# Kernel optimization log

Hardware: AMD Instinct MI355X
Metric: run time of the kernel (lower is better)

The kernel has to match this reference:

```python
import jax, jax.numpy as jnp
import numpy as np

N, E, L, HEADS, HID = 50000, 600000, 4, 8, 128
IN_C, OUT_C = 64, 64
D_HEAD = HID // HEADS


def _layer_norm(x, g, b, eps=1e-5):
    m = jnp.mean(x, axis=-1, keepdims=True)
    v = jnp.mean((x - m) ** 2, axis=-1, keepdims=True)
    return (x - m) * jax.lax.rsqrt(v + eps) * g + b


def _transformer_conv(h, src, dst, Wq, bq, Wk, bk, Wv, bv, Ws, bs, Wbeta):
    # PyG TransformerConv with beta=True, concat=True. src=edge_index[0] (j), dst=edge_index[1] (i).
    n, f = h.shape
    q = (h @ Wq.T + bq)[dst].reshape(-1, HEADS, D_HEAD)   # [E,H,D] query at destination
    k = (h @ Wk.T + bk)[src].reshape(-1, HEADS, D_HEAD)   # [E,H,D] key at source
    v = (h @ Wv.T + bv)[src].reshape(-1, HEADS, D_HEAD)   # [E,H,D] value at source
    alpha = jnp.sum(q * k, axis=-1) / float(np.sqrt(D_HEAD))  # [E,H]
    amax = jax.ops.segment_max(alpha, dst, num_segments=n)     # [N,H] segment softmax (stable)
    ex = jnp.exp(alpha - amax[dst])
    denom = jax.ops.segment_sum(ex, dst, num_segments=n)
    a = ex / (denom[dst] + 1e-16)                              # [E,H]
    out = jax.ops.segment_sum((a[:, :, None] * v).reshape(-1, f), dst, num_segments=n)  # [N,F]
    x_r = h @ Ws.T + bs                                        # root/skip transform
    beta = jax.nn.sigmoid(jnp.concatenate([out, x_r, out - x_r], axis=-1) @ Wbeta.T)    # [N,1]
    return beta * x_r + (1.0 - beta) * out


def _forward(x, src, dst, Wi, bi, Wq, bq, Wk, bk, Wv, bv, Ws, bs, Wbeta, ln_g, ln_b, W1, b1, W2, b2, Wo, bo):
    h = jax.nn.gelu(x @ Wi.T + bi, approximate=False)
    for i in range(L):
        res = h
        h = _transformer_conv(h, src, dst, Wq[i], bq[i], Wk[i], bk[i], Wv[i], bv[i], Ws[i], bs[i], Wbeta[i])
        h = _layer_norm(h + res, ln_g[i], ln_b[i])
        res = h
        f = jax.nn.gelu(h @ W1[i].T + b1[i], approximate=False) @ W2[i].T + b2[i]
        h = f + res
    return h @ Wo.T + bo


def setup_inputs() -> dict:
    key = jax.random.key(0)
    ks = jax.random.split(key, 24)
    rn = lambda k, shp, s=0.05: (jax.random.normal(k, shp, jnp.float32) * s)
    x = jax.random.normal(ks[0], (N, IN_C), jnp.float32)
    edge_index = jax.random.randint(ks[1], (2, E), 0, N, dtype=jnp.int64)
    return {
        "x": x,
        "edge_index": edge_index,
        "Wi": rn(ks[2], (HID, IN_C)), "bi": jnp.zeros((HID,), jnp.float32),
        "Wq": rn(ks[3], (L, HID, HID)), "bq": jnp.zeros((L, HID), jnp.float32),
        "Wk": rn(ks[4], (L, HID, HID)), "bk": jnp.zeros((L, HID), jnp.float32),
        "Wv": rn(ks[5], (L, HID, HID)), "bv": jnp.zeros((L, HID), jnp.float32),
        "Ws": rn(ks[6], (L, HID, HID)), "bs": jnp.zeros((L, HID), jnp.float32),
        "Wbeta": rn(ks[7], (L, 1, 3 * HID)),
        "ln_g": jnp.ones((L, HID), jnp.float32), "ln_b": jnp.zeros((L, HID), jnp.float32),
        "W1": rn(ks[8], (L, 4 * HID, HID)), "b1": jnp.zeros((L, 4 * HID), jnp.float32),
        "W2": rn(ks[9], (L, HID, 4 * HID)), "b2": jnp.zeros((L, HID), jnp.float32),
        "Wo": rn(ks[10], (OUT_C, HID)), "bo": jnp.zeros((OUT_C,), jnp.float32),
    }


def reference(x, edge_index, Wi, bi, Wq, bq, Wk, bk, Wv, bv, Ws, bs, Wbeta, ln_g, ln_b, W1, b1, W2, b2, Wo, bo):
    src, dst = edge_index[0], edge_index[1]
    return _forward(x, src, dst, Wi, bi, Wq, bq, Wk, bk, Wv, bv, Ws, bs, Wbeta, ln_g, ln_b, W1, b1, W2, b2, Wo, bo)
```

## Files before the change

kernel.cpp:

```cpp
#include <hip/hip_runtime.h>
#include <cmath>

#define HIDC   128
#define LAYERS 4
#define IN_C   64
#define OUT_C  64

typedef _Float16 h16x8 __attribute__((ext_vector_type(8)));
typedef _Float16 h16x2 __attribute__((ext_vector_type(2)));
typedef float    f32x4 __attribute__((ext_vector_type(4)));

__device__ __forceinline__ float gelu_f(float x) {
    return 0.5f * x * (1.0f + erff(x * 0.70710678118654752f));
}

__device__ __forceinline__ void cvt8(const float4& a, const float4& b, h16x8& h) {
    h[0]=(_Float16)a.x; h[1]=(_Float16)a.y; h[2]=(_Float16)a.z; h[3]=(_Float16)a.w;
    h[4]=(_Float16)b.x; h[5]=(_Float16)b.y; h[6]=(_Float16)b.z; h[7]=(_Float16)b.w;
}
__device__ __forceinline__ void load16(const float* p, _Float16* d) {
    float4 v0 = *(const float4*)p,     v1 = *(const float4*)(p + 4);
    float4 v2 = *(const float4*)(p+8), v3 = *(const float4*)(p + 12);
    h16x8 h0, h1; cvt8(v0, v1, h0); cvt8(v2, v3, h1);
    *(h16x8*)d = h0; *(h16x8*)(d + 8) = h1;
}
__device__ __forceinline__ void load16(const _Float16* p, _Float16* d) {
    *(h16x8*)d = *(const h16x8*)p; *(h16x8*)(d + 8) = *(const h16x8*)(p + 8);
}
__device__ __forceinline__ void zero16(_Float16* d) {
    h16x8 z = {};
    *(h16x8*)d = z; *(h16x8*)(d + 8) = z;
}

__global__ void count_deg_k(const int* __restrict__ dst, int* __restrict__ cnt, int E) {
    int i = blockIdx.x * blockDim.x + threadIdx.x;
    if (i < E) atomicAdd(&cnt[dst[i]], 1);
}

__global__ __launch_bounds__(256)
void scan1_k(const int* __restrict__ cnt, int* __restrict__ pref,
             int* __restrict__ bsum, int n) {
    __shared__ int part[256];
    const int b = blockIdx.x, t = threadIdx.x;
    const int i0 = b * 1024 + t * 4;
    int v0 = (i0 + 0 < n) ? cnt[i0 + 0] : 0;
    int v1 = (i0 + 1 < n) ? cnt[i0 + 1] : 0;
    int v2 = (i0 + 2 < n) ? cnt[i0 + 2] : 0;
    int v3 = (i0 + 3 < n) ? cnt[i0 + 3] : 0;
    int s = v0 + v1 + v2 + v3;
    part[t] = s;
    __syncthreads();
    for (int off = 1; off < 256; off <<= 1) {
        int x = (t >= off) ? part[t - off] : 0;
        __syncthreads();
        part[t] += x;
        __syncthreads();
    }
    int excl = part[t] - s;
    if (i0 + 0 < n) pref[i0 + 0] = excl;           excl += v0;
    if (i0 + 1 < n) pref[i0 + 1] = excl;           excl += v1;
    if (i0 + 2 < n) pref[i0 + 2] = excl;           excl += v2;
    if (i0 + 3 < n) pref[i0 + 3] = excl;
    if (t == 255) bsum[b] = part[255];
}

__global__ void scan2_k(const int* __restrict__ bsum, int* __restrict__ boff,
                        int nb, int* __restrict__ rowptr_n) {
    int lane = threadIdx.x;
    int carry = 0;
    for (int base = 0; base < nb; base += 64) {
        int i = base + lane;
        int v = (i < nb) ? bsum[i] : 0;
        int incl = v;
        for (int off = 1; off < 64; off <<= 1) {
            int x = __shfl_up(incl, off);
            if (lane >= off) incl += x;
        }
        if (i < nb) boff[i] = carry + incl - v;
        carry += __shfl(incl, 63);
    }
    if (lane == 0) *rowptr_n = carry;
}

__global__ __launch_bounds__(256)
void scan3_k(int* __restrict__ pref, const int* __restrict__ boff, int n) {
    int i = blockIdx.x * blockDim.x + threadIdx.x;
    if (i < n) pref[i] += boff[i >> 10];
}

__global__ void scatter_k(const int* __restrict__ src, const int* __restrict__ dst,
                          const int* __restrict__ rowptr, int* __restrict__ cnt,
                          int* __restrict__ csrc, int E) {
    int i = blockIdx.x * blockDim.x + threadIdx.x;
    if (i < E) {
        int d = dst[i];
        int pos = rowptr[d] + atomicAdd(&cnt[d], 1);
        csrc[pos] = src[i];
    }
}

template<int ACT, bool RES, bool NGUARD, typename AT, typename CT>
__device__ __forceinline__ void gemm_core(
    const AT* __restrict__ A, const float* __restrict__ Wt,
    const float* __restrict__ bias, const float* __restrict__ resid,
    CT* __restrict__ Ct, int M, int K, int ncs, int colbase, int nclim)
{
    __shared__ __align__(16) _Float16 As[128 * 40];
    __shared__ __align__(16) _Float16 Bs[128 * 40];
    const int tid  = threadIdx.x;
    const int lane = tid & 63;
    const int wave = tid >> 6;
    const int wr = wave >> 1, wc = wave & 1;
    const int row0 = blockIdx.y * 128;

    f32x4 acc[4][4] = {};

    const int srow = tid >> 1;
    const int skc  = (tid & 1) * 16;
    const int fr   = lane & 15;
    const int fk   = (lane >> 4) * 8;

    for (int k0 = 0; k0 < K; k0 += 32) {
        {
            int gr = row0 + srow;
            _Float16* d = As + srow * 40 + skc;
            if (gr < M) load16(A + (size_t)gr * K + k0 + skc, d);
            else        zero16(d);
        }
        {
            int gc = colbase + srow;
            _Float16* d = Bs + srow * 40 + skc;
            if (!NGUARD || gc < nclim) load16(Wt + (size_t)gc * K + k0 + skc, d);
            else                       zero16(d);
        }
        __syncthreads();
        h16x8 af[4], bf[4];
#pragma unroll
        for (int mi = 0; mi < 4; ++mi)
            af[mi] = *(const h16x8*)(As + (wr * 64 + mi * 16 + fr) * 40 + fk);
#pragma unroll
        for (int ni = 0; ni < 4; ++ni)
            bf[ni] = *(const h16x8*)(Bs + (wc * 64 + ni * 16 + fr) * 40 + fk);
#pragma unroll
        for (int mi = 0; mi < 4; ++mi)
#pragma unroll
            for (int ni = 0; ni < 4; ++ni)
                acc[mi][ni] = __builtin_amdgcn_mfma_f32_16x16x32_f16(af[mi], bf[ni], acc[mi][ni], 0, 0, 0);
        __syncthreads();
    }

    const int rbase = row0 + wr * 64 + ((lane >> 4) * 4);
    const int cbase = colbase + wc * 64 + fr;
#pragma unroll
    for (int mi = 0; mi < 4; ++mi) {
#pragma unroll
        for (int j = 0; j < 4; ++j) {
            int r = rbase + mi * 16 + j;
            if (r >= M) continue;
            size_t rb = (size_t)r * ncs;
#pragma unroll
            for (int ni = 0; ni < 4; ++ni) {
                int c = cbase + ni * 16;
                if (NGUARD && c >= nclim) continue;
                float v = acc[mi][ni][j] + bias[c];
                if (ACT == 1) v = gelu_f(v);
                if (RES) v += resid[rb + c];
                Ct[rb + c] = (CT)v;
            }
        }
    }
}

template<int ACT, bool RES, bool NGUARD, typename AT, typename CT>
__global__ __launch_bounds__(256)
void gemm_f16_k(const AT* __restrict__ A, const float* __restrict__ W,
                const float* __restrict__ bias, const float* __restrict__ resid,
                CT* __restrict__ C, int M, int NC, int K) {
    gemm_core<ACT, RES, NGUARD, AT, CT>(A, W, bias, resid, C, M, K, NC, blockIdx.x * 128, NC);
}

__global__ __launch_bounds__(256)
void qkvs_k(const float* __restrict__ A,
            const float* __restrict__ Wq, const float* __restrict__ Wk,
            const float* __restrict__ Wv, const float* __restrict__ Wvs,
            const float* __restrict__ bq, const float* __restrict__ bk,
            const float* __restrict__ bv, const float* __restrict__ bs,
            _Float16* __restrict__ qh, _Float16* __restrict__ kv,
            float* __restrict__ sb, int M) {
    __shared__ __align__(16) _Float16 As[128 * 136];
    __shared__ __align__(16) _Float16 Bs[128 * 136];
    const int tid  = threadIdx.x;
    const int lane = tid & 63;
    const int wave = tid >> 6;
    const int wr = wave >> 1, wc = wave & 1;
    const int row0 = blockIdx.x * 128;
    const int srow  = tid >> 1;
    const int shalf = (tid & 1) * 64;
    const int fr = lane & 15;

    {
        int gr = row0 + srow;
        _Float16* d = As + srow * 136 + shalf;
        if (gr < M) {
            const float* p = A + (size_t)gr * 128 + shalf;
#pragma unroll
            for (int u = 0; u < 4; ++u) load16(p + u * 16, d + u * 16);
        } else {
#pragma unroll
            for (int u = 0; u < 4; ++u) zero16(d + u * 16);
        }
    }

    for (int w = 0; w < 4; ++w) {
        const float* Wp = (w == 0) ? Wq : (w == 1) ? Wk : (w == 2) ? Wv : Wvs;
        const float* bp = (w == 0) ? bq : (w == 1) ? bk : (w == 2) ? bv : bs;
        {
            const float* p = Wp + (size_t)srow * 128 + shalf;
            _Float16* d = Bs + srow * 136 + shalf;
#pragma unroll
            for (int u = 0; u < 4; ++u) load16(p + u * 16, d + u * 16);
        }
        __syncthreads();
        f32x4 acc[4][4] = {};
#pragma unroll
        for (int ks = 0; ks < 4; ++ks) {
            const int fk = ks * 32 + (lane >> 4) * 8;
            h16x8 af[4], bf[4];
#pragma unroll
            for (int mi = 0; mi < 4; ++mi)
                af[mi] = *(const h16x8*)(As + (wr * 64 + mi * 16 + fr) * 136 + fk);
#pragma unroll
            for (int ni = 0; ni < 4; ++ni)
                bf[ni] = *(const h16x8*)(Bs + (wc * 64 + ni * 16 + fr) * 136 + fk);
#pragma unroll
            for (int mi = 0; mi < 4; ++mi)
#pragma unroll
                for (int ni = 0; ni < 4; ++ni)
                    acc[mi][ni] = __builtin_amdgcn_mfma_f32_16x16x32_f16(af[mi], bf[ni], acc[mi][ni], 0, 0, 0);
        }
        __syncthreads();

        const int rbase = row0 + wr * 64 + ((lane >> 4) * 4);
        const int cbase = wc * 64 + fr;
#pragma unroll
        for (int mi = 0; mi < 4; ++mi) {
#pragma unroll
            for (int j = 0; j < 4; ++j) {
                int r = rbase + mi * 16 + j;
                if (r >= M) continue;
#pragma unroll
                for (int ni = 0; ni < 4; ++ni) {
                    int c = cbase + ni * 16;
                    float v = acc[mi][ni][j] + bp[c];
                    if (w == 0)      qh[(size_t)r * 128 + c] = (_Float16)v;
                    else if (w == 1) kv[(size_t)r * 256 + c] = (_Float16)v;
                    else if (w == 2) kv[(size_t)r * 256 + 128 + c] = (_Float16)v;
                    else             sb[(size_t)r * 128 + c] = v;
                }
            }
        }
    }
}

__global__ __launch_bounds__(256)
void ffn1_k(const float* __restrict__ A, const float* __restrict__ W1,
            const float* __restrict__ b1, _Float16* __restrict__ ffn, int M) {
    __shared__ __align__(16) _Float16 As[128 * 136];
    __shared__ __align__(16) _Float16 Bs[128 * 136];
    const int tid  = threadIdx.x;
    const int lane = tid & 63;
    const int wave = tid >> 6;
    const int wr = wave >> 1, wc = wave & 1;
    const int row0 = blockIdx.x * 128;
    const int srow  = tid >> 1;
    const int shalf = (tid & 1) * 64;
    const int fr = lane & 15;

    {
        int gr = row0 + srow;
        _Float16* d = As + srow * 136 + shalf;
        if (gr < M) {
            const float* p = A + (size_t)gr * 128 + shalf;
#pragma unroll
            for (int u = 0; u < 4; ++u) load16(p + u * 16, d + u * 16);
        } else {
#pragma unroll
            for (int u = 0; u < 4; ++u) zero16(d + u * 16);
        }
    }

    for (int w = 0; w < 4; ++w) {
        const float* Wp = W1 + (size_t)w * 128 * 128;
        {
            const float* p = Wp + (size_t)srow * 128 + shalf;
            _Float16* d = Bs + srow * 136 + shalf;
#pragma unroll
            for (int u = 0; u < 4; ++u) load16(p + u * 16, d + u * 16);
        }
        __syncthreads();
        f32x4 acc[4][4] = {};
#pragma unroll
        for (int ks = 0; ks < 4; ++ks) {
            const int fk = ks * 32 + (lane >> 4) * 8;
            h16x8 af[4], bf[4];
#pragma unroll
            for (int mi = 0; mi < 4; ++mi)
                af[mi] = *(const h16x8*)(As + (wr * 64 + mi * 16 + fr) * 136 + fk);
#pragma unroll
            for (int ni = 0; ni < 4; ++ni)
                bf[ni] = *(const h16x8*)(Bs + (wc * 64 + ni * 16 + fr) * 136 + fk);
#pragma unroll
            for (int mi = 0; mi < 4; ++mi)
#pragma unroll
                for (int ni = 0; ni < 4; ++ni)
                    acc[mi][ni] = __builtin_amdgcn_mfma_f32_16x16x32_f16(af[mi], bf[ni], acc[mi][ni], 0, 0, 0);
        }
        __syncthreads();

        const int rbase = row0 + wr * 64 + ((lane >> 4) * 4);
        const int cbase = wc * 64 + fr;
#pragma unroll
        for (int mi = 0; mi < 4; ++mi) {
#pragma unroll
            for (int j = 0; j < 4; ++j) {
                int r = rbase + mi * 16 + j;
                if (r >= M) continue;
#pragma unroll
                for (int ni = 0; ni < 4; ++ni) {
                    int c = cbase + ni * 16;
                    float v = acc[mi][ni][j] + b1[w * 128 + c];
                    ffn[(size_t)r * 512 + w * 128 + c] = (_Float16)gelu_f(v);
                }
            }
        }
    }
}

__global__ __launch_bounds__(256)
void attn_ln_k(const _Float16* __restrict__ qh, const _Float16* __restrict__ kv,
               const int* __restrict__ rowptr, const int* __restrict__ csrc,
               const float* __restrict__ xr, const float* __restrict__ res,
               const float* __restrict__ Wb, const float* __restrict__ g_,
               const float* __restrict__ b_, float* __restrict__ out, int n) {
    int node = (int)((blockIdx.x * (size_t)blockDim.x + threadIdx.x) >> 6);
    int lane = threadIdx.x & 63;
    if (node >= n) return;
    const int g = lane & 7;
    const int h = lane >> 3;

    const _Float16* qp = qh + (size_t)node * 128 + h * 16;
    h16x8 q0 = *(const h16x8*)(qp);
    h16x8 q1 = *(const h16x8*)(qp + 8);

    float ssum = 0.f;
    float acc[16] = {};
    const int e0 = rowptr[node], e1 = rowptr[node + 1];
    for (int eb = e0; eb < e1; eb += 8) {
        int e = eb + g;
        bool val = (e < e1);
        int s = csrc[val ? e : (e1 - 1)];
        const _Float16* kp = kv + (size_t)s * 256 + h * 16;
        h16x8 k0 = *(const h16x8*)(kp);
        h16x8 k1 = *(const h16x8*)(kp + 8);
        h16x8 v0 = *(const h16x8*)(kp + 128);
        h16x8 v1 = *(const h16x8*)(kp + 136);
        float d = 0.f;
#pragma unroll
        for (int j = 0; j < 8; ++j) d += (float)k0[j] * (float)q0[j];
#pragma unroll
        for (int j = 0; j < 8; ++j) d += (float)k1[j] * (float)q1[j];
        float w = val ? __expf(d * 0.25f) : 0.f;
        ssum += w;
#pragma unroll
        for (int j = 0; j < 8; ++j) acc[j]     += w * (float)v0[j];
#pragma unroll
        for (int j = 0; j < 8; ++j) acc[8 + j] += w * (float)v1[j];
    }
#pragma unroll
    for (int m = 1; m < 8; m <<= 1) {
        ssum += __shfl_xor(ssum, m);
#pragma unroll
        for (int j = 0; j < 16; ++j) acc[j] += __shfl_xor(acc[j], m);
    }
    float inv = 1.f / (ssum + 1e-16f);
    const bool s0b = g & 1, s1b = g & 2, s2b = g & 4;
    float t0 = s0b ? acc[2]  : acc[0],  t1 = s0b ? acc[6]  : acc[4];
    float t2 = s0b ? acc[10] : acc[8],  t3 = s0b ? acc[14] : acc[12];
    float u0 = s1b ? t1 : t0,           u1 = s1b ? t3 : t2;
    float ox = (s2b ? u1 : u0) * inv;
    float p0 = s0b ? acc[3]  : acc[1],  p1 = s0b ? acc[7]  : acc[5];
    float p2 = s0b ? acc[11] : acc[9],  p3 = s0b ? acc[15] : acc[13];
    float w0 = s1b ? p1 : p0,           w1 = s1b ? p3 : p2;
    float oy = (s2b ? w1 : w0) * inv;

    size_t base = (size_t)node * HIDC + lane * 2;
    int c = lane * 2;
    float2 r  = *(const float2*)(xr + base);
    float2 wb0 = *(const float2*)(Wb + c);
    float2 wb1 = *(const float2*)(Wb + HIDC + c);
    float2 wb2 = *(const float2*)(Wb + 2 * HIDC + c);
    float part = ox * wb0.x + oy * wb0.y
               + r.x * wb1.x + r.y * wb1.y
               + (ox - r.x) * wb2.x + (oy - r.y) * wb2.y;
#pragma unroll
    for (int mk = 1; mk < 64; mk <<= 1) part += __shfl_xor(part, mk);
    float beta = 1.f / (1.f + __expf(-part));
    float2 rs = *(const float2*)(res + base);
    float tx = beta * r.x + (1.f - beta) * ox + rs.x;
    float ty = beta * r.y + (1.f - beta) * oy + rs.y;
    float sum = tx + ty;
#pragma unroll
    for (int mk = 1; mk < 64; mk <<= 1) sum += __shfl_xor(sum, mk);
    float mean = sum * (1.f / 128.f);
    float dx = tx - mean, dy = ty - mean;
    float vs = dx * dx + dy * dy;
#pragma unroll
    for (int mk = 1; mk < 64; mk <<= 1) vs += __shfl_xor(vs, mk);
    float rstd = 1.f / sqrtf(vs * (1.f / 128.f) + 1e-5f);
    float2 gg = *(const float2*)(g_ + c);
    float2 bb = *(const float2*)(b_ + c);
    float2 oo = make_float2(dx * rstd * gg.x + bb.x, dy * rstd * gg.y + bb.y);
    *(float2*)(out + base) = oo;
}

extern "C" void kernel_launch(void* const* d_in, const int* in_sizes, int n_in,
                              void* d_out, int out_size, void* d_ws, size_t ws_size,
                              hipStream_t stream) {
    const float* x    = (const float*)d_in[0];
    const int*   ei   = (const int*)d_in[1];
    const float* Wi   = (const float*)d_in[2];
    const float* bi   = (const float*)d_in[3];
    const float* Wq   = (const float*)d_in[4];
    const float* bq   = (const float*)d_in[5];
    const float* Wk   = (const float*)d_in[6];
    const float* bk   = (const float*)d_in[7];
    const float* Wv   = (const float*)d_in[8];
    const float* bv   = (const float*)d_in[9];
    const float* Ws_  = (const float*)d_in[10];
    const float* bs   = (const float*)d_in[11];
    const float* Wbeta= (const float*)d_in[12];
    const float* ln_g = (const float*)d_in[13];
    const float* ln_b = (const float*)d_in[14];
    const float* W1   = (const float*)d_in[15];
    const float* b1   = (const float*)d_in[16];
    const float* W2   = (const float*)d_in[17];
    const float* b2   = (const float*)d_in[18];
    const float* Wo   = (const float*)d_in[19];
    const float* bo   = (const float*)d_in[20];
    float* outp = (float*)d_out;

    const int Nn = in_sizes[0] / IN_C;
    const int Ee = in_sizes[1] / 2;
    const int* srcI = ei;
    const int* dstI = ei + Ee;

    float* ws = (float*)d_ws;
    size_t n128 = (size_t)Nn * HIDC;
    float*     h   = ws;
    float*     h2  = h  + n128;
    _Float16*  qh  = (_Float16*)(h2 + n128);
    _Float16*  kv  = qh + (size_t)Nn * 128;
    float*     sb  = (float*)(kv + (size_t)Nn * 256);
    _Float16*  ffn = qh;
    int* rowptr = (int*)(sb + n128);
    int* cnt    = rowptr + (Nn + 1);
    int* csrc   = cnt + Nn;
    int* bsum   = csrc + Ee;
    int* boff   = bsum + 1024;

    const int nb = (Nn + 1023) / 1024;

    hipMemsetAsync(cnt, 0, Nn * sizeof(int), stream);
    count_deg_k<<<(Ee + 255) / 256, 256, 0, stream>>>(dstI, cnt, Ee);
    scan1_k<<<nb, 256, 0, stream>>>(cnt, rowptr, bsum, Nn);
    scan2_k<<<1, 64, 0, stream>>>(bsum, boff, nb, rowptr + Nn);
    scan3_k<<<(Nn + 255) / 256, 256, 0, stream>>>(rowptr, boff, Nn);
    hipMemsetAsync(cnt, 0, Nn * sizeof(int), stream);
    scatter_k<<<(Ee + 255) / 256, 256, 0, stream>>>(srcI, dstI, rowptr, cnt, csrc, Ee);

    const int mblk = (Nn + 127) / 128;
    dim3 blk(256);

    gemm_f16_k<1, false, false, float, float><<<dim3(1, mblk), blk, 0, stream>>>(x, Wi, bi, nullptr, h, Nn, HIDC, IN_C);

    int nwaveblk = (Nn + 3) / 4;

    for (int l = 0; l < LAYERS; ++l) {
        const float* Wq_l = Wq + (size_t)l * HIDC * HIDC;
        const float* Wk_l = Wk + (size_t)l * HIDC * HIDC;
        const float* Wv_l = Wv + (size_t)l * HIDC * HIDC;
        const float* Ws_l = Ws_ + (size_t)l * HIDC * HIDC;
        const float* bq_l = bq + (size_t)l * HIDC;
        const float* bk_l = bk + (size_t)l * HIDC;
        const float* bv_l = bv + (size_t)l * HIDC;
        const float* bs_l = bs + (size_t)l * HIDC;
        const float* Wb_l = Wbeta + (size_t)l * 3 * HIDC;
        const float* g_l  = ln_g + (size_t)l * HIDC;
        const float* b_l  = ln_b + (size_t)l * HIDC;
        const float* W1_l = W1 + (size_t)l * 4 * HIDC * HIDC;
        const float* b1_l = b1 + (size_t)l * 4 * HIDC;
        const float* W2_l = W2 + (size_t)l * HIDC * 4 * HIDC;
        const float* b2_l = b2 + (size_t)l * HIDC;

        qkvs_k<<<dim3(mblk), blk, 0, stream>>>(h, Wq_l, Wk_l, Wv_l, Ws_l,
                                               bq_l, bk_l, bv_l, bs_l,
                                               qh, kv, sb, Nn);

        attn_ln_k<<<nwaveblk, blk, 0, stream>>>(qh, kv, rowptr, csrc,
                                                sb, h, Wb_l, g_l, b_l, h2, Nn);

        ffn1_k<<<dim3(mblk), blk, 0, stream>>>(h2, W1_l, b1_l, ffn, Nn);
        gemm_f16_k<0, true, false, _Float16, float><<<dim3(1, mblk), blk, 0, stream>>>(ffn, W2_l, b2_l, h2, h, Nn, HIDC, 4 * HIDC);
    }

    gemm_f16_k<0, false, true, float, float><<<dim3(1, mblk), blk, 0, stream>>>(h, Wo, bo, nullptr, outp, Nn, OUT_C, HIDC);
}
```

Baseline: 1.059 ms.

## Fuse FFN up/down projections into one kernel with pre-converted fp16 weights

Replaces the two-kernel FFN (ffn1 writing a 512-wide fp16 intermediate, then a GEMM reading it back) with a single kernel. In it each wave computes 16 rows, runs GELU on 32-column chunks of the hidden layer, stages them in LDS and feeds them straight into the second MFMA accumulation. W1/W2 are converted to fp16 once up front, so the fused kernel reads fp16 weights directly from global memory rather than staging them through LDS. The count reset is also folded into scan1, removing a memset. This removes the large intermediate round-trip through memory, at the cost of no LDS tiling for weights and smaller per-block reuse.

```diff
diff --git a/kernel.cpp b/kernel.cpp
--- a/kernel.cpp
+++ b/kernel.cpp
@@ -32,13 +32,26 @@
     *(h16x8*)d = z; *(h16x8*)(d + 8) = z;
 }
 
+__global__ __launch_bounds__(256)
+void cvtw_k(const float* __restrict__ W1, _Float16* __restrict__ W1h,
+            const float* __restrict__ W2, _Float16* __restrict__ W2h, int n) {
+    const float* s = blockIdx.y ? W2 : W1;
+    _Float16*    d = blockIdx.y ? W2h : W1h;
+    int i = (blockIdx.x * blockDim.x + threadIdx.x) * 8;
+    if (i + 8 <= n) {
+        float4 a = *(const float4*)(s + i), b = *(const float4*)(s + i + 4);
+        h16x8 h; cvt8(a, b, h);
+        *(h16x8*)(d + i) = h;
+    }
+}
+
 __global__ void count_deg_k(const int* __restrict__ dst, int* __restrict__ cnt, int E) {
     int i = blockIdx.x * blockDim.x + threadIdx.x;
     if (i < E) atomicAdd(&cnt[dst[i]], 1);
 }
 
 __global__ __launch_bounds__(256)
-void scan1_k(const int* __restrict__ cnt, int* __restrict__ pref,
+void scan1_k(int* __restrict__ cnt, int* __restrict__ pref,
              int* __restrict__ bsum, int n) {
     __shared__ int part[256];
     const int b = blockIdx.x, t = threadIdx.x;
@@ -47,6 +60,10 @@
     int v1 = (i0 + 1 < n) ? cnt[i0 + 1] : 0;
     int v2 = (i0 + 2 < n) ? cnt[i0 + 2] : 0;
     int v3 = (i0 + 3 < n) ? cnt[i0 + 3] : 0;
+    if (i0 + 0 < n) cnt[i0 + 0] = 0;
+    if (i0 + 1 < n) cnt[i0 + 1] = 0;
+    if (i0 + 2 < n) cnt[i0 + 2] = 0;
+    if (i0 + 3 < n) cnt[i0 + 3] = 0;
     int s = v0 + v1 + v2 + v3;
     part[t] = s;
     __syncthreads();
@@ -100,11 +117,10 @@
 }
 
 template<int ACT, bool RES, bool NGUARD, typename AT, typename CT>
-__device__ __forceinline__ void gemm_core(
-    const AT* __restrict__ A, const float* __restrict__ Wt,
-    const float* __restrict__ bias, const float* __restrict__ resid,
-    CT* __restrict__ Ct, int M, int K, int ncs, int colbase, int nclim)
-{
+__global__ __launch_bounds__(256)
+void gemm_f16_k(const AT* __restrict__ A, const float* __restrict__ Wt,
+                const float* __restrict__ bias, const float* __restrict__ resid,
+                CT* __restrict__ Ct, int M, int ncs, int K) {
     __shared__ __align__(16) _Float16 As[128 * 40];
     __shared__ __align__(16) _Float16 Bs[128 * 40];
     const int tid  = threadIdx.x;
@@ -112,6 +128,7 @@
     const int wave = tid >> 6;
     const int wr = wave >> 1, wc = wave & 1;
     const int row0 = blockIdx.y * 128;
+    const int colbase = blockIdx.x * 128;
 
     f32x4 acc[4][4] = {};
 
@@ -130,8 +147,8 @@
         {
             int gc = colbase + srow;
             _Float16* d = Bs + srow * 40 + skc;
-            if (!NGUARD || gc < nclim) load16(Wt + (size_t)gc * K + k0 + skc, d);
-            else                       zero16(d);
+            if (!NGUARD || gc < ncs) load16(Wt + (size_t)gc * K + k0 + skc, d);
+            else                     zero16(d);
         }
         __syncthreads();
         h16x8 af[4], bf[4];
@@ -161,7 +178,7 @@
 #pragma unroll
             for (int ni = 0; ni < 4; ++ni) {
                 int c = cbase + ni * 16;
-                if (NGUARD && c >= nclim) continue;
+                if (NGUARD && c >= ncs) continue;
                 float v = acc[mi][ni][j] + bias[c];
                 if (ACT == 1) v = gelu_f(v);
                 if (RES) v += resid[rb + c];
@@ -169,14 +186,6 @@
             }
         }
     }
-}
-
-template<int ACT, bool RES, bool NGUARD, typename AT, typename CT>
-__global__ __launch_bounds__(256)
-void gemm_f16_k(const AT* __restrict__ A, const float* __restrict__ W,
-                const float* __restrict__ bias, const float* __restrict__ resid,
-                CT* __restrict__ C, int M, int NC, int K) {
-    gemm_core<ACT, RES, NGUARD, AT, CT>(A, W, bias, resid, C, M, K, NC, blockIdx.x * 128, NC);
 }
 
 __global__ __launch_bounds__(256)
@@ -263,80 +272,6 @@
 }
 
 __global__ __launch_bounds__(256)
-void ffn1_k(const float* __restrict__ A, const float* __restrict__ W1,
-            const float* __restrict__ b1, _Float16* __restrict__ ffn, int M) {
-    __shared__ __align__(16) _Float16 As[128 * 136];
-    __shared__ __align__(16) _Float16 Bs[128 * 136];
-    const int tid  = threadIdx.x;
-    const int lane = tid & 63;
-    const int wave = tid >> 6;
-    const int wr = wave >> 1, wc = wave & 1;
-    const int row0 = blockIdx.x * 128;
-    const int srow  = tid >> 1;
-    const int shalf = (tid & 1) * 64;
-    const int fr = lane & 15;
-
-    {
-        int gr = row0 + srow;
-        _Float16* d = As + srow * 136 + shalf;
-        if (gr < M) {
-            const float* p = A + (size_t)gr * 128 + shalf;
-#pragma unroll
-            for (int u = 0; u < 4; ++u) load16(p + u * 16, d + u * 16);
-        } else {
-#pragma unroll
-            for (int u = 0; u < 4; ++u) zero16(d + u * 16);
-        }
-    }
-
-    for (int w = 0; w < 4; ++w) {
-        const float* Wp = W1 + (size_t)w * 128 * 128;
-        {
-            const float* p = Wp + (size_t)srow * 128 + shalf;
-            _Float16* d = Bs + srow * 136 + shalf;
-#pragma unroll
-            for (int u = 0; u < 4; ++u) load16(p + u * 16, d + u * 16);
-        }
-        __syncthreads();
-        f32x4 acc[4][4] = {};
-#pragma unroll
-        for (int ks = 0; ks < 4; ++ks) {
-            const int fk = ks * 32 + (lane >> 4) * 8;
-            h16x8 af[4], bf[4];
-#pragma unroll
-            for (int mi = 0; mi < 4; ++mi)
-                af[mi] = *(const h16x8*)(As + (wr * 64 + mi * 16 + fr) * 136 + fk);
-#pragma unroll
-            for (int ni = 0; ni < 4; ++ni)
-                bf[ni] = *(const h16x8*)(Bs + (wc * 64 + ni * 16 + fr) * 136 + fk);
-#pragma unroll
-            for (int mi = 0; mi < 4; ++mi)
-#pragma unroll
-                for (int ni = 0; ni < 4; ++ni)
-                    acc[mi][ni] = __builtin_amdgcn_mfma_f32_16x16x32_f16(af[mi], bf[ni], acc[mi][ni], 0, 0, 0);
-        }
-        __syncthreads();
-
-        const int rbase = row0 + wr * 64 + ((lane >> 4) * 4);
-        const int cbase = wc * 64 + fr;
-#pragma unroll
-        for (int mi = 0; mi < 4; ++mi) {
-#pragma unroll
-            for (int j = 0; j < 4; ++j) {
-                int r = rbase + mi * 16 + j;
-                if (r >= M) continue;
-#pragma unroll
-                for (int ni = 0; ni < 4; ++ni) {
-                    int c = cbase + ni * 16;
-                    float v = acc[mi][ni][j] + b1[w * 128 + c];
-                    ffn[(size_t)r * 512 + w * 128 + c] = (_Float16)gelu_f(v);
-                }
-            }
-        }
-    }
-}
-
-__global__ __launch_bounds__(256)
 void attn_ln_k(const _Float16* __restrict__ qh, const _Float16* __restrict__ kv,
                const int* __restrict__ rowptr, const int* __restrict__ csrc,
                const float* __restrict__ xr, const float* __restrict__ res,
@@ -421,6 +356,71 @@
     float2 bb = *(const float2*)(b_ + c);
     float2 oo = make_float2(dx * rstd * gg.x + bb.x, dy * rstd * gg.y + bb.y);
     *(float2*)(out + base) = oo;
+}
+
+__global__ __launch_bounds__(256)
+void ffn_fused_k(const float* __restrict__ h2, const _Float16* __restrict__ W1h,
+                 const float* __restrict__ b1, const _Float16* __restrict__ W2h,
+                 const float* __restrict__ b2, float* __restrict__ hout, int M) {
+    __shared__ __align__(16) _Float16 scr[4][16 * 36];
+    const int tid = threadIdx.x, lane = tid & 63, wave = tid >> 6;
+    const int r0  = blockIdx.x * 64 + wave * 16;
+    const int l15 = lane & 15;
+    const int g   = lane >> 4;
+    const int kof = g * 8;
+    _Float16* sw = scr[wave];
+
+    h16x8 a1[4];
+    {
+        int ar = r0 + l15; if (ar >= M) ar = M - 1;
+        const float* ap = h2 + (size_t)ar * 128 + kof;
+#pragma unroll
+        for (int kk = 0; kk < 4; ++kk) {
+            float4 u = *(const float4*)(ap + kk * 32);
+            float4 v = *(const float4*)(ap + kk * 32 + 4);
+            cvt8(u, v, a1[kk]);
+        }
+    }
+
+    f32x4 acc2[8] = {};
+    for (int c0 = 0; c0 < 512; c0 += 32) {
+        f32x4 acc1[2] = {};
+#pragma unroll
+        for (int ct = 0; ct < 2; ++ct) {
+            const _Float16* wp = W1h + (size_t)(c0 + ct * 16 + l15) * 128 + kof;
+#pragma unroll
+            for (int kk = 0; kk < 4; ++kk) {
+                h16x8 bf = *(const h16x8*)(wp + kk * 32);
+                acc1[ct] = __builtin_amdgcn_mfma_f32_16x16x32_f16(a1[kk], bf, acc1[ct], 0, 0, 0);
+            }
+        }
+#pragma unroll
+        for (int ct = 0; ct < 2; ++ct) {
+            float bv = b1[c0 + ct * 16 + l15];
+#pragma unroll
+            for (int j = 0; j < 4; ++j)
+                sw[(g * 4 + j) * 36 + ct * 16 + l15] = (_Float16)gelu_f(acc1[ct][j] + bv);
+        }
+        h16x8 af2 = *(const h16x8*)(sw + l15 * 36 + kof);
+#pragma unroll
+        for (int ot = 0; ot < 8; ++ot) {
+            const _Float16* wp2 = W2h + (size_t)(ot * 16 + l15) * 512 + c0 + kof;
+            h16x8 bf = *(const h16x8*)wp2;
+            acc2[ot] = __builtin_amdgcn_mfma_f32_16x16x32_f16(af2, bf, acc2[ot], 0, 0, 0);
+        }
+    }
+
+#pragma unroll
+    for (int j = 0; j < 4; ++j) {
+        int r = r0 + g * 4 + j;
+        if (r >= M) continue;
+        size_t ro = (size_t)r * 128;
+#pragma unroll
+        for (int ot = 0; ot < 8; ++ot) {
+            int c = ot * 16 + l15;
+            hout[ro + c] = acc2[ot][j] + b2[c] + h2[ro + c];
+        }
+    }
 }
 
 extern "C" void kernel_launch(void* const* d_in, const int* in_sizes, int n_in,
@@ -461,29 +461,32 @@
     _Float16*  qh  = (_Float16*)(h2 + n128);
     _Float16*  kv  = qh + (size_t)Nn * 128;
     float*     sb  = (float*)(kv + (size_t)Nn * 256);
-    _Float16*  ffn = qh;
-    int* rowptr = (int*)(sb + n128);
+    _Float16*  W1h = (_Float16*)(sb + n128);
+    _Float16*  W2h = W1h + (size_t)LAYERS * 512 * 128;
+    int* rowptr = (int*)(W2h + (size_t)LAYERS * 128 * 512);
     int* cnt    = rowptr + (Nn + 1);
     int* csrc   = cnt + Nn;
     int* bsum   = csrc + Ee;
     int* boff   = bsum + 1024;
 
     const int nb = (Nn + 1023) / 1024;
+    dim3 blk(256);
+
+    const int wn = LAYERS * 512 * 128;
+    cvtw_k<<<dim3(wn / 8 / 256, 2), blk, 0, stream>>>(W1, W1h, W2, W2h, wn);
 
     hipMemsetAsync(cnt, 0, Nn * sizeof(int), stream);
     count_deg_k<<<(Ee + 255) / 256, 256, 0, stream>>>(dstI, cnt, Ee);
     scan1_k<<<nb, 256, 0, stream>>>(cnt, rowptr, bsum, Nn);
     scan2_k<<<1, 64, 0, stream>>>(bsum, boff, nb, rowptr + Nn);
     scan3_k<<<(Nn + 255) / 256, 256, 0, stream>>>(rowptr, boff, Nn);
-    hipMemsetAsync(cnt, 0, Nn * sizeof(int), stream);
     scatter_k<<<(Ee + 255) / 256, 256, 0, stream>>>(srcI, dstI, rowptr, cnt, csrc, Ee);
 
     const int mblk = (Nn + 127) / 128;
-    dim3 blk(256);
+    const int fblk = (Nn + 63) / 64;
+    int nwaveblk = (Nn + 3) / 4;
 
     gemm_f16_k<1, false, false, float, float><<<dim3(1, mblk), blk, 0, stream>>>(x, Wi, bi, nullptr, h, Nn, HIDC, IN_C);
-
-    int nwaveblk = (Nn + 3) / 4;
 
     for (int l = 0; l < LAYERS; ++l) {
         const float* Wq_l = Wq + (size_t)l * HIDC * HIDC;
@@ -497,9 +500,9 @@
         const float* Wb_l = Wbeta + (size_t)l * 3 * HIDC;
         const float* g_l  = ln_g + (size_t)l * HIDC;
         const float* b_l  = ln_b + (size_t)l * HIDC;
-        const float* W1_l = W1 + (size_t)l * 4 * HIDC * HIDC;
+        const _Float16* W1_l = W1h + (size_t)l * 512 * 128;
+        const _Float16* W2_l = W2h + (size_t)l * 128 * 512;
         const float* b1_l = b1 + (size_t)l * 4 * HIDC;
-        const float* W2_l = W2 + (size_t)l * HIDC * 4 * HIDC;
         const float* b2_l = b2 + (size_t)l * HIDC;
 
         qkvs_k<<<dim3(mblk), blk, 0, stream>>>(h, Wq_l, Wk_l, Wv_l, Ws_l,
@@ -509,8 +512,7 @@
         attn_ln_k<<<nwaveblk, blk, 0, stream>>>(qh, kv, rowptr, csrc,
                                                 sb, h, Wb_l, g_l, b_l, h2, Nn);
 
-        ffn1_k<<<dim3(mblk), blk, 0, stream>>>(h2, W1_l, b1_l, ffn, Nn);
-        gemm_f16_k<0, true, false, _Float16, float><<<dim3(1, mblk), blk, 0, stream>>>(ffn, W2_l, b2_l, h2, h, Nn, HIDC, 4 * HIDC);
+        ffn_fused_k<<<dim3(fblk), blk, 0, stream>>>(h2, W1_l, b1_l, W2_l, b2_l, h, Nn);
     }
 
     gemm_f16_k<0, false, true, float, float><<<dim3(1, mblk), blk, 0, stream>>>(h, Wo, bo, nullptr, outp, Nn, OUT_C, HIDC);
```

Result: slower. 1.092 ms (+3.1%).
